# Performance work log

Measured on AMD Instinct MI355X. Metric: run time of the kernel, lower is better.

The kernel has to match this reference:

```python
import jax, jax.numpy as jnp
import numpy as np

N_HEAD = 16  # matches init_kwargs
LN_EPS = 1e-5


def setup_inputs() -> dict:
    key = jax.random.key(0)
    k0, k1, k2 = jax.random.split(key, 3)
    S, B, D = 2048, 2, 1024
    N, Dh = N_HEAD, D // N_HEAD
    h = jax.random.normal(k0, (S, B, D), dtype=jnp.float32)
    # causal mask, True = masked; source's dim==3 branch: shape [qlen, klen, batch]
    causal = jnp.triu(jnp.ones((S, S), dtype=bool), k=1)
    attn_mask = jnp.broadcast_to(causal[:, :, None], (S, S, B))
    W_qkv = jax.random.normal(k1, (D, 3 * N * Dh), dtype=jnp.float32) * (1.0 / np.sqrt(D))
    W_o = jax.random.normal(k2, (N * Dh, D), dtype=jnp.float32) * (1.0 / np.sqrt(N * Dh))
    gamma = jnp.ones((D,), dtype=jnp.float32)
    beta = jnp.zeros((D,), dtype=jnp.float32)
    return {"h": h, "attn_mask": attn_mask, "W_qkv": W_qkv, "W_o": W_o,
            "gamma": gamma, "beta": beta}


def reference(h, attn_mask, W_qkv, W_o, gamma, beta):
    # h: [S, B, D] (seq, batch, d_model) -- Transformer-XL layout
    S, B, D = h.shape
    N = N_HEAD
    Dh = W_o.shape[0] // N
    scale = 1.0 / np.sqrt(Dh)

    qkv = h @ W_qkv                                   # [S, B, 3*N*Dh]
    q, k, v = jnp.split(qkv, 3, axis=-1)
    q = q.reshape(S, B, N, Dh)
    k = k.reshape(S, B, N, Dh)
    v = v.reshape(S, B, N, Dh)

    # attention scores: [i, j, b, n]
    score = jnp.einsum('ibnd,jbnd->ijbn', q, k) * scale
    # mask (dim==3 branch of source): attn_mask [i, j, b] -> [i, j, b, 1]
    score = jnp.where(attn_mask[:, :, :, None], -jnp.inf, score)
    prob = jax.nn.softmax(score, axis=1)              # softmax over key axis j

    attn_vec = jnp.einsum('ijbn,jbnd->ibnd', prob, v).reshape(S, B, N * Dh)
    attn_out = attn_vec @ W_o                         # [S, B, D]

    # residual + LayerNorm (biased variance, like torch.nn.LayerNorm)
    x = h + attn_out
    mu = jnp.mean(x, axis=-1, keepdims=True)
    var = jnp.mean(jnp.square(x - mu), axis=-1, keepdims=True)
    out = (x - mu) * jax.lax.rsqrt(var + LN_EPS) * gamma + beta
    return out
```

## Files before the change

### kernel.cpp

```cpp
#include <hip/hip_runtime.h>

typedef unsigned short u16;
typedef unsigned int u32;
typedef __attribute__((ext_vector_type(8))) __bf16 bf16x8;
typedef __attribute__((ext_vector_type(4))) float f32x4;
typedef __attribute__((ext_vector_type(8))) unsigned short u16x8;
typedef __attribute__((ext_vector_type(4))) unsigned short u16x4;
typedef __attribute__((ext_vector_type(2))) unsigned int u32x2;
typedef __attribute__((ext_vector_type(4))) unsigned int u32x4;

#if defined(__has_builtin)
#if __has_builtin(__builtin_amdgcn_permlane32_swap) && __has_builtin(__builtin_amdgcn_permlane16_swap)
#define USE_PERMLANE 1
#endif
#endif
#ifndef USE_PERMLANE
#define USE_PERMLANE 0
#endif

__device__ __forceinline__ u16 f2bf(float f) {
    u32 u = __builtin_bit_cast(u32, f);
    u += 0x7fffu + ((u >> 16) & 1u);
    return (u16)(u >> 16);
}

__device__ __forceinline__ float fexp2(float x) {
#if __has_builtin(__builtin_amdgcn_exp2f)
    return __builtin_amdgcn_exp2f(x);
#else
    return exp2f(x);
#endif
}

__device__ __forceinline__ float frcp(float x) {
#if __has_builtin(__builtin_amdgcn_rcpf)
    return __builtin_amdgcn_rcpf(x);
#else
    return 1.0f / x;
#endif
}

#define GL16(gp, lp) __builtin_amdgcn_global_load_lds(                           \
    (const __attribute__((address_space(1))) void*)(gp),                          \
    (__attribute__((address_space(3))) void*)(lp), 16, 0, 0)

__global__ __launch_bounds__(256) void conv_h_kernel(const float* __restrict__ h,
                                                     u16* __restrict__ hb) {
    int i = blockIdx.x * 256 + threadIdx.x;
    float4 v = ((const float4*)h)[i];
    u16x4 o = { f2bf(v.x), f2bf(v.y), f2bf(v.z), f2bf(v.w) };
    ((u16x4*)hb)[i] = o;
}

__global__ __launch_bounds__(256) void conv_wt_kernel(const float* __restrict__ W,
                                                      u16* __restrict__ Wt,
                                                      int R, int C,
                                                      int scale_rows, float scale) {
    __shared__ float tile[32][33];
    int t = threadIdx.x;
    int r = t >> 3, c4 = (t & 7) * 4;
    int gx = blockIdx.x * 32, gy = blockIdx.y * 32;
    float4 v = *(const float4*)&W[(size_t)(gy + r) * C + gx + c4];
    tile[r][c4 + 0] = v.x; tile[r][c4 + 1] = v.y;
    tile[r][c4 + 2] = v.z; tile[r][c4 + 3] = v.w;
    __syncthreads();
    float sc = (gx + r < scale_rows) ? scale : 1.0f;
    u16x4 o = { f2bf(tile[c4 + 0][r] * sc), f2bf(tile[c4 + 1][r] * sc),
                f2bf(tile[c4 + 2][r] * sc), f2bf(tile[c4 + 3][r] * sc) };
    *(u16x4*)&Wt[(size_t)(gx + r) * R + gy + c4] = o;
}

__global__ __launch_bounds__(512, 2) void gemm1_8ph_kernel(
        const u16* __restrict__ A, const u16* __restrict__ Bt,
        u16* __restrict__ Cb, int M, int N, int K) {
    __shared__ u16 alds[2][2][8192];
    __shared__ u16 blds[2][2][8192];
    const int t = threadIdx.x;
    const int lane = t & 63;
    const int wave = t >> 6;
    const int wm = wave >> 2;
    const int wn = wave & 3;
    const int li = lane & 15, lg = lane >> 4;

    const int nwg = (int)gridDim.x;
    const int lin = (int)blockIdx.x;
    const int swz = (lin & 7) * (nwg >> 3) + (lin >> 3);
    const int mt = M >> 8;
    const int m0 = (swz % mt) << 8;
    const int n0 = (swz / mt) << 8;

    const int srow = lane >> 2;
    const int sslot = ((lane & 3) ^ ((lane >> 2) & 3)) * 8;
    const u16* gAb = A + (size_t)(m0 + wave * 32 + srow) * K + sslot;
    const u16* gBb = Bt + (size_t)(n0 + wave * 32 + srow) * K + sslot;
    const int ldst = wave * 1024;

#define STAGE_A1(buf, ks, kt)                                                    \
    { GL16(gAb + (size_t)(kt) * 64 + (ks) * 32, &alds[buf][ks][ldst]);           \
      GL16(gAb + (size_t)16 * K + (size_t)(kt) * 64 + (ks) * 32,                 \
           &alds[buf][ks][ldst + 512]); }
#define STAGE_B1(buf, ks, kt)                                                    \
    { GL16(gBb + (size_t)(kt) * 64 + (ks) * 32, &blds[buf][ks][ldst]);           \
      GL16(gBb + (size_t)16 * K + (size_t)(kt) * 64 + (ks) * 32,                 \
           &blds[buf][ks][ldst + 512]); }

    const int rslot = (lg ^ (li & 3)) * 8;
#define READ_A(buf, ks, mh)                                                      \
    _Pragma("unroll") for (int m = 0; m < 4; ++m)                                \
        af[m] = *(const bf16x8*)&alds[buf][ks][(wm * 128 + (mh) * 64 + m * 16 + li) * 32 + rslot];
#define READ_B(buf, ks)                                                          \
    _Pragma("unroll") for (int n = 0; n < 4; ++n)                                \
        bfr[n] = *(const bf16x8*)&blds[buf][ks][(wn * 64 + n * 16 + li) * 32 + rslot];
#define MFMA16(mh)                                                               \
    _Pragma("unroll") for (int m = 0; m < 4; ++m)                                \
        _Pragma("unroll") for (int n = 0; n < 4; ++n)                            \
            acc[(mh) * 4 + m][n] = __builtin_amdgcn_mfma_f32_16x16x32_bf16(      \
                af[m], bfr[n], acc[(mh) * 4 + m][n], 0, 0, 0);

#define PH_BAR() __builtin_amdgcn_s_barrier()
#define PH_MFMA(mh)                                                              \
    PH_BAR();                                                                    \
    __builtin_amdgcn_s_setprio(1); MFMA16(mh); __builtin_amdgcn_s_setprio(0);    \
    PH_BAR();
#define VMCNT4() asm volatile("s_waitcnt vmcnt(4)" ::: "memory")

    f32x4 acc[8][4] = {};
    bf16x8 af[4], bfr[4];

    STAGE_A1(0, 0, 0); STAGE_B1(0, 0, 0);
    STAGE_A1(0, 1, 0); STAGE_B1(0, 1, 0);
    STAGE_A1(1, 0, 1); STAGE_B1(1, 0, 1);
    VMCNT4();
    PH_BAR();

    const int NIT = K >> 7;
    for (int i = 0; i < NIT; ++i) {
        const int t1 = 2 * i + 1, t2 = 2 * i + 2, t3 = 2 * i + 3;
        const bool more = (i + 1 < NIT);
        READ_A(0, 0, 0); READ_B(0, 0);
        STAGE_A1(1, 1, t1);
        PH_MFMA(0);
        READ_A(0, 0, 1);
        STAGE_B1(1, 1, t1);
        PH_MFMA(1);
        READ_A(0, 1, 0); READ_B(0, 1);
        if (more) STAGE_A1(0, 0, t2);
        PH_MFMA(0);
        READ_A(0, 1, 1);
        if (more) STAGE_B1(0, 0, t2);
        VMCNT4();
        PH_MFMA(1);
        READ_A(1, 0, 0); READ_B(1, 0);
        if (more) STAGE_A1(0, 1, t2);
        PH_MFMA(0);
        READ_A(1, 0, 1);
        if (more) STAGE_B1(0, 1, t2);
        PH_MFMA(1);
        READ_A(1, 1, 0); READ_B(1, 1);
        if (more) STAGE_A1(1, 0, t3);
        PH_MFMA(0);
        READ_A(1, 1, 1);
        if (more) STAGE_B1(1, 0, t3);
        VMCNT4();
        PH_MFMA(1);
    }

#pragma unroll
    for (int mr = 0; mr < 8; ++mr)
#pragma unroll
        for (int nr = 0; nr < 4; ++nr)
#pragma unroll
            for (int rr = 0; rr < 4; ++rr) {
                int row = m0 + wm * 128 + mr * 16 + lg * 4 + rr;
                int col = n0 + wn * 64 + nr * 16 + li;
                Cb[(size_t)row * N + col] = f2bf(acc[mr][nr][rr]);
            }
#undef STAGE_A1
#undef STAGE_B1
#undef READ_A
#undef READ_B
#undef MFMA16
#undef PH_BAR
#undef PH_MFMA
#undef VMCNT4
}

template <int MODE>
__global__ __launch_bounds__(256) void gemm_bt_kernel(
        const u16* __restrict__ A, const u16* __restrict__ Bt,
        u16* __restrict__ Cb, const float* __restrict__ H, float* __restrict__ X,
        int M, int N, int K) {
    constexpr int LDT = 40;
    __shared__ u16 alds[2][128 * LDT];
    __shared__ u16 blds[2][128 * LDT];
    const int t = threadIdx.x;
    const int lane = t & 63;
    const int wave = t >> 6;
    const int wm = wave >> 1, wn = wave & 1;
    const int m0 = blockIdx.x * 128;
    const int n0 = blockIdx.y * 128;
    const int nk = K >> 5;

    const int srow = t >> 1;
    const int sch = (t & 1) * 2;
    const u16* ga = A + (size_t)(m0 + srow) * K + sch * 8;
    const u16* gb = Bt + (size_t)(n0 + srow) * K + sch * 8;
    const int wo = srow * LDT + sch * 8;

    u16x8 ra0 = *(const u16x8*)(ga);
    u16x8 ra1 = *(const u16x8*)(ga + 8);
    u16x8 rb0 = *(const u16x8*)(gb);
    u16x8 rb1 = *(const u16x8*)(gb + 8);
    *(u16x8*)&alds[0][wo] = ra0;  *(u16x8*)&alds[0][wo + 8] = ra1;
    *(u16x8*)&blds[0][wo] = rb0;  *(u16x8*)&blds[0][wo + 8] = rb1;

    f32x4 acc[4][4] = {};
    const int ko = (lane >> 4) * 8;
    const int arow_base = wm * 64 + (lane & 15);
    const int brow_base = wn * 64 + (lane & 15);

    int cur = 0;
    for (int kt = 0; kt < nk; ++kt) {
        __syncthreads();
        if (kt + 1 < nk) {
            const u16* gan = ga + (kt + 1) * 32;
            const u16* gbn = gb + (kt + 1) * 32;
            ra0 = *(const u16x8*)(gan);
            ra1 = *(const u16x8*)(gan + 8);
            rb0 = *(const u16x8*)(gbn);
            rb1 = *(const u16x8*)(gbn + 8);
        }
        bf16x8 afrag[4], bfrag[4];
#pragma unroll
        for (int m = 0; m < 4; ++m)
            afrag[m] = *(const bf16x8*)&alds[cur][(arow_base + m * 16) * LDT + ko];
#pragma unroll
        for (int n = 0; n < 4; ++n)
            bfrag[n] = *(const bf16x8*)&blds[cur][(brow_base + n * 16) * LDT + ko];
#pragma unroll
        for (int m = 0; m < 4; ++m)
#pragma unroll
            for (int n = 0; n < 4; ++n)
                acc[m][n] = __builtin_amdgcn_mfma_f32_16x16x32_bf16(afrag[m], bfrag[n],
                                                                   acc[m][n], 0, 0, 0);
        if (kt + 1 < nk) {
            *(u16x8*)&alds[cur ^ 1][wo] = ra0;  *(u16x8*)&alds[cur ^ 1][wo + 8] = ra1;
            *(u16x8*)&blds[cur ^ 1][wo] = rb0;  *(u16x8*)&blds[cur ^ 1][wo + 8] = rb1;
        }
        cur ^= 1;
    }

#pragma unroll
    for (int m = 0; m < 4; ++m)
#pragma unroll
        for (int n = 0; n < 4; ++n)
#pragma unroll
            for (int r = 0; r < 4; ++r) {
                int row = m0 + wm * 64 + m * 16 + (lane >> 4) * 4 + r;
                int col = n0 + wn * 64 + n * 16 + (lane & 15);
                size_t idx = (size_t)row * N + col;
                if (MODE == 0) Cb[idx] = f2bf(acc[m][n][r]);
                else           X[idx] = acc[m][n][r] + H[idx];
            }
}

__global__ __launch_bounds__(256) void transpose_v_kernel(const u16* __restrict__ qkvb,
                                                          u16* __restrict__ vt) {
    __shared__ u16 tl[64][72];
    const int t = threadIdx.x;
    const int p = blockIdx.y;
    const int nn = p >> 1, b = p & 1;
    const int s0 = blockIdx.x * 64;
    const int r = t >> 2;
    const int ch = (t & 3) * 2;
    const u16* g = qkvb + ((size_t)(s0 + r) * 2 + b) * 3072 + 2048 + nn * 64;
    *(u16x8*)&tl[r][ch * 8]     = *(const u16x8*)(g + ch * 8);
    *(u16x8*)&tl[r][ch * 8 + 8] = *(const u16x8*)(g + ch * 8 + 8);
    __syncthreads();
    const int dh = t >> 2;
    const int sc = (t & 3) * 2;
    u16* o = vt + ((size_t)p * 64 + dh) * 2048 + s0;
#pragma unroll
    for (int q = 0; q < 2; ++q) {
        int scq = sc + q;
        u16x8 v;
#pragma unroll
        for (int j = 0; j < 8; ++j) v[j] = tl[scq * 8 + j][dh];
        *(u16x8*)(o + scq * 8) = v;
    }
}

__global__ __launch_bounds__(256) void attn_kernel(const u16* __restrict__ qkvb,
                                                   const u16* __restrict__ vt,
                                                   u16* __restrict__ attnb) {
    constexpr int LKT = 72;
    __shared__ u16 klds[2][64 * LKT];
    __shared__ u16 vlds[2][64 * LKT];
#if !USE_PERMLANE
    __shared__ u16 plds[4][16 * LKT];
#endif
    const int t = threadIdx.x;
    const int lane = t & 63;
    const int w = t >> 6;
    const int bid = blockIdx.x;
    const int g = bid >> 5;
    const int sq = g & 7, jq = g >> 3;
    const int qt = (jq == 0) ? (31 - sq) : (jq == 1) ? (16 + sq)
                 : (jq == 2) ? (15 - sq) : sq;
    const int p = bid & 31;
    const int nn = p >> 1, b = p & 1;
    const int i0 = qt * 64;

    const int li = lane & 15;
    const int lg = lane >> 4;

    const int qrow = i0 + w * 16 + li;
    const u16* qg = qkvb + ((size_t)qrow * 2 + b) * 3072 + nn * 64 + lg * 8;
    bf16x8 qa0 = *(const bf16x8*)(qg);
    bf16x8 qa1 = *(const bf16x8*)(qg + 32);

    f32x4 o[4] = {};
    float mrun = -3.0e38f;
    float lrun = 0.f;

    const int srow = t >> 2;
    const int sch = (t & 3) * 2;
    const u16* kg = qkvb + 1024 + nn * 64 + sch * 8;
    const u16* vg = vt + ((size_t)p * 64 + srow) * 2048 + sch * 8;
    const int swo = srow * LKT + sch * 8;

    const int nt = qt + 1;
    u16x8 k0, k1, v0, v1;
    {
        const u16* kgp = kg + ((size_t)srow * 2 + b) * 3072;
        k0 = *(const u16x8*)(kgp);  k1 = *(const u16x8*)(kgp + 8);
        v0 = *(const u16x8*)(vg);   v1 = *(const u16x8*)(vg + 8);
    }
    *(u16x8*)&klds[0][swo] = k0;  *(u16x8*)&klds[0][swo + 8] = k1;
    *(u16x8*)&vlds[0][swo] = v0;  *(u16x8*)&vlds[0][swo + 8] = v1;
    __syncthreads();

    for (int jt = 0; jt < nt; ++jt) {
        const int buf = jt & 1;
        if (jt + 1 < nt) {
            const u16* kgp = kg + ((size_t)(jt * 64 + 64 + srow) * 2 + b) * 3072;
            k0 = *(const u16x8*)(kgp);  k1 = *(const u16x8*)(kgp + 8);
            const u16* vgp = vg + jt * 64 + 64;
            v0 = *(const u16x8*)(vgp);  v1 = *(const u16x8*)(vgp + 8);
        }

        f32x4 st[4];
        __builtin_amdgcn_s_setprio(1);
#pragma unroll
        for (int cf = 0; cf < 4; ++cf) {
            bf16x8 kb0 = *(const bf16x8*)&klds[buf][(cf * 16 + li) * LKT + lg * 8];
            bf16x8 kb1 = *(const bf16x8*)&klds[buf][(cf * 16 + li) * LKT + 32 + lg * 8];
            f32x4 z = {};
            z = __builtin_amdgcn_mfma_f32_16x16x32_bf16(kb0, qa0, z, 0, 0, 0);
            z = __builtin_amdgcn_mfma_f32_16x16x32_bf16(kb1, qa1, z, 0, 0, 0);
            st[cf] = z;
        }
        __builtin_amdgcn_s_setprio(0);

        if (jt == qt) {
            const int it = w * 16 + li;
#pragma unroll
            for (int cf = 0; cf < 4; ++cf)
#pragma unroll
                for (int r = 0; r < 4; ++r) {
                    int jl = cf * 16 + lg * 4 + r;
                    if (jl > it) st[cf][r] = -3.0e38f;
                }
        }

        float mloc = st[0][0];
#pragma unroll
        for (int cf = 0; cf < 4; ++cf)
#pragma unroll
            for (int r = 0; r < 4; ++r) mloc = fmaxf(mloc, st[cf][r]);
        mloc = fmaxf(mloc, __shfl_xor(mloc, 16, 64));
        mloc = fmaxf(mloc, __shfl_xor(mloc, 32, 64));

        if (__any(mloc > mrun + 8.0f)) {
            float mnew = fmaxf(mrun, mloc);
            float alpha = fexp2(mrun - mnew);
            lrun *= alpha;
            mrun = mnew;
#pragma unroll
            for (int r = 0; r < 4; ++r) {
                float ar = __shfl(alpha, lg * 4 + r, 64);
#pragma unroll
                for (int cf = 0; cf < 4; ++cf) o[cf][r] *= ar;
            }
        }

#if USE_PERMLANE
        float rsum = 0.f;
        u32 wv[4][2];
#pragma unroll
        for (int cf = 0; cf < 4; ++cf)
#pragma unroll
            for (int rr = 0; rr < 2; ++rr) {
                float p0 = fexp2(st[cf][2 * rr] - mrun);
                float p1 = fexp2(st[cf][2 * rr + 1] - mrun);
                rsum += p0 + p1;
                u32 wres;
                asm("v_cvt_pk_bf16_f32 %0, %1, %2" : "=v"(wres) : "v"(p0), "v"(p1));
                wv[cf][rr] = wres;
            }
        rsum += __shfl_xor(rsum, 16, 64);
        rsum += __shfl_xor(rsum, 32, 64);
        lrun += rsum;

        __builtin_amdgcn_s_setprio(1);
#pragma unroll
        for (int ks = 0; ks < 2; ++ks) {
            u32x2 sa = __builtin_amdgcn_permlane32_swap(wv[2 * ks][0], wv[2 * ks + 1][0], false, false);
            u32x2 fa = __builtin_amdgcn_permlane16_swap(sa[0], sa[1], false, false);
            u32x2 sb = __builtin_amdgcn_permlane32_swap(wv[2 * ks][1], wv[2 * ks + 1][1], false, false);
            u32x2 fb = __builtin_amdgcn_permlane16_swap(sb[0], sb[1], false, false);
            u32x4 fw = { fa[0], fb[0], fa[1], fb[1] };
            bf16x8 pa = __builtin_bit_cast(bf16x8, fw);
#pragma unroll
            for (int cf = 0; cf < 4; ++cf) {
                bf16x8 vb = *(const bf16x8*)&vlds[buf][(cf * 16 + li) * LKT + ks * 32 + lg * 8];
                o[cf] = __builtin_amdgcn_mfma_f32_16x16x32_bf16(pa, vb, o[cf], 0, 0, 0);
            }
        }
        __builtin_amdgcn_s_setprio(0);
#else
        float rsum = 0.f;
#pragma unroll
        for (int cf = 0; cf < 4; ++cf) {
            u16x4 pw;
#pragma unroll
            for (int r = 0; r < 4; ++r) {
                float pv = fexp2(st[cf][r] - mrun);
                rsum += pv;
                pw[r] = f2bf(pv);
            }
            *(u16x4*)&plds[w][li * LKT + cf * 16 + lg * 4] = pw;
        }
        rsum += __shfl_xor(rsum, 16, 64);
        rsum += __shfl_xor(rsum, 32, 64);
        lrun += rsum;

        asm volatile("s_waitcnt lgkmcnt(0)" ::: "memory");
        __builtin_amdgcn_sched_barrier(0);

#pragma unroll
        for (int ks = 0; ks < 2; ++ks) {
            bf16x8 pa = *(const bf16x8*)&plds[w][li * LKT + ks * 32 + lg * 8];
#pragma unroll
            for (int cf = 0; cf < 4; ++cf) {
                bf16x8 vb = *(const bf16x8*)&vlds[buf][(cf * 16 + li) * LKT + ks * 32 + lg * 8];
                o[cf] = __builtin_amdgcn_mfma_f32_16x16x32_bf16(pa, vb, o[cf], 0, 0, 0);
            }
        }
#endif

        if (jt + 1 < nt) {
            *(u16x8*)&klds[buf ^ 1][swo] = k0;  *(u16x8*)&klds[buf ^ 1][swo + 8] = k1;
            *(u16x8*)&vlds[buf ^ 1][swo] = v0;  *(u16x8*)&vlds[buf ^ 1][swo + 8] = v1;
        }
        __syncthreads();
    }

    float rinv = frcp(lrun);
#pragma unroll
    for (int r = 0; r < 4; ++r) {
        float rv = __shfl(rinv, lg * 4 + r, 64);
        int srowg = i0 + w * 16 + lg * 4 + r;
        u16* og = attnb + ((size_t)srowg * 2 + b) * 1024 + nn * 64;
#pragma unroll
        for (int cf = 0; cf < 4; ++cf)
            og[cf * 16 + li] = f2bf(o[cf][r] * rv);
    }
}

__global__ __launch_bounds__(256) void ln_kernel(const float* __restrict__ X,
                                                 const float* __restrict__ gamma,
                                                 const float* __restrict__ beta,
                                                 float* __restrict__ out) {
    __shared__ float red[8];
    const int t = threadIdx.x;
    const int row = blockIdx.x;
    float4 v = ((const float4*)(X + (size_t)row * 1024))[t];
    float s = v.x + v.y + v.z + v.w;
#pragma unroll
    for (int off = 1; off < 64; off <<= 1) s += __shfl_xor(s, off, 64);
    if ((t & 63) == 0) red[t >> 6] = s;
    __syncthreads();
    float mu = (red[0] + red[1] + red[2] + red[3]) * (1.f / 1024.f);
    float dx = v.x - mu, dy = v.y - mu, dz = v.z - mu, dw = v.w - mu;
    float q = dx * dx + dy * dy + dz * dz + dw * dw;
#pragma unroll
    for (int off = 1; off < 64; off <<= 1) q += __shfl_xor(q, off, 64);
    if ((t & 63) == 0) red[4 + (t >> 6)] = q;
    __syncthreads();
    float var = (red[4] + red[5] + red[6] + red[7]) * (1.f / 1024.f);
    float rs = rsqrtf(var + 1e-5f);
    float4 g = ((const float4*)gamma)[t];
    float4 bt = ((const float4*)beta)[t];
    float4 o;
    o.x = dx * rs * g.x + bt.x;
    o.y = dy * rs * g.y + bt.y;
    o.z = dz * rs * g.z + bt.z;
    o.w = dw * rs * g.w + bt.w;
    ((float4*)(out + (size_t)row * 1024))[t] = o;
}

extern "C" void kernel_launch(void* const* d_in, const int* in_sizes, int n_in,
                              void* d_out, int out_size, void* d_ws, size_t ws_size,
                              hipStream_t stream) {
    const float* h     = (const float*)d_in[0];
    const float* Wqkv  = (const float*)d_in[2];
    const float* Wo    = (const float*)d_in[3];
    const float* gamma = (const float*)d_in[4];
    const float* beta  = (const float*)d_in[5];
    float* out = (float*)d_out;

    char* ws = (char*)d_ws;
    u16*   hb    = (u16*)(ws);
    u16*   wqkvt = (u16*)(ws + 8388608);
    u16*   wot   = (u16*)(ws + 14680064);
    u16*   qkvb  = (u16*)(ws + 16777216);
    u16*   vt    = (u16*)(ws + 41943040);
    u16*   attnb = (u16*)(ws + 50331648);
    float* xbuf  = (float*)(ws + 58720256);

    const float qscale = 0.125f * 1.44269504088896f;

    conv_h_kernel<<<4096, 256, 0, stream>>>(h, hb);
    conv_wt_kernel<<<dim3(96, 32), 256, 0, stream>>>(Wqkv, wqkvt, 1024, 3072, 1024, qscale);
    conv_wt_kernel<<<dim3(32, 32), 256, 0, stream>>>(Wo, wot, 1024, 1024, 0, 1.0f);
    gemm1_8ph_kernel<<<192, 512, 0, stream>>>(hb, wqkvt, qkvb, 4096, 3072, 1024);
    transpose_v_kernel<<<dim3(32, 32), 256, 0, stream>>>(qkvb, vt);
    attn_kernel<<<1024, 256, 0, stream>>>(qkvb, vt, attnb);
    gemm_bt_kernel<1><<<dim3(32, 8), 256, 0, stream>>>(attnb, wot, nullptr, h, xbuf,
                                                       4096, 1024, 1024);
    ln_kernel<<<4096, 256, 0, stream>>>(xbuf, gamma, beta, out);
}
```

Baseline: 124.7 us.

## Retune QKV GEMM pipeline waits, XCD tile mapping and LDS swizzle

The QKV GEMM now maps the 192 workgroups to tiles so each XCD covers a 4x6 block of output tiles. The goal is better L2 reuse of A and B rows within an XCD. The loop is hard-coded to K=1024 with a peeled final iteration, and the global-load wait is relaxed to vmcnt(8) at more points, so more loads stay in flight. The LDS XOR swizzle now uses different row bits to reduce bank conflicts. The kernel now hard-codes shapes and grid size, and the relaxed waits depend on the exact order in which loads are issued for correctness.

```diff
diff --git a/kernel.cpp b/kernel.cpp
--- a/kernel.cpp
+++ b/kernel.cpp
@@ -82,15 +82,15 @@
     const int wn = wave & 3;
     const int li = lane & 15, lg = lane >> 4;
 
-    const int nwg = (int)gridDim.x;
     const int lin = (int)blockIdx.x;
-    const int swz = (lin & 7) * (nwg >> 3) + (lin >> 3);
-    const int mt = M >> 8;
-    const int m0 = (swz % mt) << 8;
-    const int n0 = (swz / mt) << 8;
+    const int xcd = lin & 7;
+    const int c = lin >> 3;
+    const int mi = c & 3, ni = c >> 2;
+    const int m0 = ((xcd & 3) * 4 + mi) << 8;
+    const int n0 = (((xcd >> 2) * 6) + ni) << 8;
 
     const int srow = lane >> 2;
-    const int sslot = ((lane & 3) ^ ((lane >> 2) & 3)) * 8;
+    const int sslot = ((lane & 3) ^ ((lane >> 3) & 3)) * 8;
     const u16* gAb = A + (size_t)(m0 + wave * 32 + srow) * K + sslot;
     const u16* gBb = Bt + (size_t)(n0 + wave * 32 + srow) * K + sslot;
     const int ldst = wave * 1024;
@@ -104,7 +104,7 @@
       GL16(gBb + (size_t)16 * K + (size_t)(kt) * 64 + (ks) * 32,                 \
            &blds[buf][ks][ldst + 512]); }
 
-    const int rslot = (lg ^ (li & 3)) * 8;
+    const int rslot = (lg ^ ((li >> 1) & 3)) * 8;
 #define READ_A(buf, ks, mh)                                                      \
     _Pragma("unroll") for (int m = 0; m < 4; ++m)                                \
         af[m] = *(const bf16x8*)&alds[buf][ks][(wm * 128 + (mh) * 64 + m * 16 + li) * 32 + rslot];
@@ -116,13 +116,13 @@
         _Pragma("unroll") for (int n = 0; n < 4; ++n)                            \
             acc[(mh) * 4 + m][n] = __builtin_amdgcn_mfma_f32_16x16x32_bf16(      \
                 af[m], bfr[n], acc[(mh) * 4 + m][n], 0, 0, 0);
-
-#define PH_BAR() __builtin_amdgcn_s_barrier()
 #define PH_MFMA(mh)                                                              \
-    PH_BAR();                                                                    \
+    __builtin_amdgcn_s_barrier();                                                \
     __builtin_amdgcn_s_setprio(1); MFMA16(mh); __builtin_amdgcn_s_setprio(0);    \
-    PH_BAR();
-#define VMCNT4() asm volatile("s_waitcnt vmcnt(4)" ::: "memory")
+    __builtin_amdgcn_s_barrier();
+#define W8() asm volatile("s_waitcnt vmcnt(8)" ::: "memory")
+#define W4() asm volatile("s_waitcnt vmcnt(4)" ::: "memory")
+#define W0() asm volatile("s_waitcnt vmcnt(0)" ::: "memory")
 
     f32x4 acc[8][4] = {};
     bf16x8 af[4], bfr[4];
@@ -130,39 +130,29 @@
     STAGE_A1(0, 0, 0); STAGE_B1(0, 0, 0);
     STAGE_A1(0, 1, 0); STAGE_B1(0, 1, 0);
     STAGE_A1(1, 0, 1); STAGE_B1(1, 0, 1);
-    VMCNT4();
-    PH_BAR();
-
-    const int NIT = K >> 7;
-    for (int i = 0; i < NIT; ++i) {
+    W4();
+    __builtin_amdgcn_s_barrier();
+
+    for (int i = 0; i < 7; ++i) {
         const int t1 = 2 * i + 1, t2 = 2 * i + 2, t3 = 2 * i + 3;
-        const bool more = (i + 1 < NIT);
-        READ_A(0, 0, 0); READ_B(0, 0);
-        STAGE_A1(1, 1, t1);
-        PH_MFMA(0);
-        READ_A(0, 0, 1);
-        STAGE_B1(1, 1, t1);
-        PH_MFMA(1);
-        READ_A(0, 1, 0); READ_B(0, 1);
-        if (more) STAGE_A1(0, 0, t2);
-        PH_MFMA(0);
-        READ_A(0, 1, 1);
-        if (more) STAGE_B1(0, 0, t2);
-        VMCNT4();
-        PH_MFMA(1);
-        READ_A(1, 0, 0); READ_B(1, 0);
-        if (more) STAGE_A1(0, 1, t2);
-        PH_MFMA(0);
-        READ_A(1, 0, 1);
-        if (more) STAGE_B1(0, 1, t2);
-        PH_MFMA(1);
-        READ_A(1, 1, 0); READ_B(1, 1);
-        if (more) STAGE_A1(1, 0, t3);
-        PH_MFMA(0);
-        READ_A(1, 1, 1);
-        if (more) STAGE_B1(1, 0, t3);
-        VMCNT4();
-        PH_MFMA(1);
+        READ_A(0, 0, 0); READ_B(0, 0); STAGE_A1(1, 1, t1);        PH_MFMA(0);
+        READ_A(0, 0, 1);               STAGE_B1(1, 1, t1); W8();  PH_MFMA(1);
+        READ_A(0, 1, 0); READ_B(0, 1); STAGE_A1(0, 0, t2);        PH_MFMA(0);
+        READ_A(0, 1, 1);               STAGE_B1(0, 0, t2); W8();  PH_MFMA(1);
+        READ_A(1, 0, 0); READ_B(1, 0); STAGE_A1(0, 1, t2);        PH_MFMA(0);
+        READ_A(1, 0, 1);               STAGE_B1(0, 1, t2); W8();  PH_MFMA(1);
+        READ_A(1, 1, 0); READ_B(1, 1); STAGE_A1(1, 0, t3);        PH_MFMA(0);
+        READ_A(1, 1, 1);               STAGE_B1(1, 0, t3); W8();  PH_MFMA(1);
+    }
+    {
+        READ_A(0, 0, 0); READ_B(0, 0); STAGE_A1(1, 1, 15);        PH_MFMA(0);
+        READ_A(0, 0, 1);               STAGE_B1(1, 1, 15); W8();  PH_MFMA(1);
+        READ_A(0, 1, 0); READ_B(0, 1);                            PH_MFMA(0);
+        READ_A(0, 1, 1);                                   W4();  PH_MFMA(1);
+        READ_A(1, 0, 0); READ_B(1, 0);                            PH_MFMA(0);
+        READ_A(1, 0, 1);                                   W0();  PH_MFMA(1);
+        READ_A(1, 1, 0); READ_B(1, 1);                            PH_MFMA(0);
+        READ_A(1, 1, 1);                                          PH_MFMA(1);
     }
 
 #pragma unroll
@@ -180,15 +170,15 @@
 #undef READ_A
 #undef READ_B
 #undef MFMA16
-#undef PH_BAR
 #undef PH_MFMA
-#undef VMCNT4
-}
-
-template <int MODE>
+#undef W8
+#undef W4
+#undef W0
+}
+
 __global__ __launch_bounds__(256) void gemm_bt_kernel(
         const u16* __restrict__ A, const u16* __restrict__ Bt,
-        u16* __restrict__ Cb, const float* __restrict__ H, float* __restrict__ X,
+        const float* __restrict__ H, float* __restrict__ X,
         int M, int N, int K) {
     constexpr int LDT = 40;
     __shared__ u16 alds[2][128 * LDT];
@@ -259,8 +249,7 @@
                 int row = m0 + wm * 64 + m * 16 + (lane >> 4) * 4 + r;
                 int col = n0 + wn * 64 + n * 16 + (lane & 15);
                 size_t idx = (size_t)row * N + col;
-                if (MODE == 0) Cb[idx] = f2bf(acc[m][n][r]);
-                else           X[idx] = acc[m][n][r] + H[idx];
+                X[idx] = acc[m][n][r] + H[idx];
             }
 }
 
@@ -537,7 +526,6 @@
     gemm1_8ph_kernel<<<192, 512, 0, stream>>>(hb, wqkvt, qkvb, 4096, 3072, 1024);
     transpose_v_kernel<<<dim3(32, 32), 256, 0, stream>>>(qkvb, vt);
     attn_kernel<<<1024, 256, 0, stream>>>(qkvb, vt, attnb);
-    gemm_bt_kernel<1><<<dim3(32, 8), 256, 0, stream>>>(attnb, wot, nullptr, h, xbuf,
-                                                       4096, 1024, 1024);
+    gemm_bt_kernel<<<dim3(32, 8), 256, 0, stream>>>(attnb, wot, h, xbuf, 4096, 1024, 1024);
     ln_kernel<<<4096, 256, 0, stream>>>(xbuf, gamma, beta, out);
 }
```

Measured after the change: 122.7 us. Within noise of the previous version (-1.5%).
